# Performance work log

Measured on AMD Instinct MI355X. Metric: run time of the kernel, lower is better.

The kernel has to match this reference:

```python
import jax, jax.numpy as jnp
import numpy as np

VARIANCE = (0.1, 0.2)
NUM_CLASSES = 81
NEGPOS_RATIO = 3
THRESH = 0.5


def point_form(b):
    # cxcywh -> xyxy
    return jnp.concatenate([b[:, :2] - b[:, 2:] / 2, b[:, :2] + b[:, 2:] / 2], axis=1)


def iou_jaccard(box1, box2):
    # box1: [G,4] xyxy, box2: [P,4] xyxy -> [G,P]
    lt = jnp.maximum(box1[:, None, :2], box2[None, :, :2])
    rb = jnp.minimum(box1[:, None, 2:], box2[None, :, 2:])
    wh = jnp.clip(rb - lt, 0.0)
    inter = wh[..., 0] * wh[..., 1]
    a1 = ((box1[:, 2] - box1[:, 0]) * (box1[:, 3] - box1[:, 1]))[:, None]
    a2 = ((box2[:, 2] - box2[:, 0]) * (box2[:, 3] - box2[:, 1]))[None, :]
    return inter / (a1 + a2 - inter)


def encode(matched, priors):
    # matched: [P,4] xyxy gt per prior; priors: [P,4] cxcywh
    cxcy = (matched[:, :2] + matched[:, 2:]) / 2 - priors[:, :2]
    cxcy = cxcy / (priors[:, 2:] * VARIANCE[0])
    wh = jnp.log((matched[:, 2:] - matched[:, :2]) / priors[:, 2:]) / VARIANCE[1]
    return jnp.concatenate([cxcy, wh], axis=1)


def assign_one(gt_box, gt_class, priors):
    ov = iou_jaccard(gt_box, point_form(priors))  # [G,P]
    best_iou = ov.max(axis=0)                      # [P]
    best_gt = ov.argmax(axis=0)                    # [P]
    best_prior = ov.argmax(axis=1)                 # [G]
    best_iou = best_iou.at[best_prior].set(2.0)    # force-keep each gt's best prior
    loc_t = encode(gt_box[best_gt], priors)
    cls = gt_class[best_gt] + 1
    cls = jnp.where(best_iou < THRESH, 0, cls)
    return loc_t, cls


def setup_inputs() -> dict:
    key = jax.random.key(0)
    ks = jax.random.split(key, 7)
    B, P, C, G = 64, 8732, NUM_CLASSES, 16
    loc_p = jax.random.normal(ks[0], (B, P, 4), jnp.float32)
    class_p = jax.random.normal(ks[1], (B, P, C), jnp.float32)
    p_cxcy = jax.random.uniform(ks[2], (P, 2), jnp.float32, 0.05, 0.95)
    p_wh = jax.random.uniform(ks[3], (P, 2), jnp.float32, 0.05, 0.5)
    priors = jnp.concatenate([p_cxcy, p_wh], axis=1)
    xy1 = jax.random.uniform(ks[4], (B, G, 2), jnp.float32, 0.0, 0.6)
    wh = jax.random.uniform(ks[5], (B, G, 2), jnp.float32, 0.05, 0.35)
    gt_box = jnp.concatenate([xy1, xy1 + wh], axis=-1)
    gt_class = jax.random.randint(ks[6], (B, G), 0, C - 1, jnp.int32)
    return {"loc_p": loc_p, "class_p": class_p, "priors": priors,
            "gt_box": gt_box, "gt_class": gt_class}


def reference(loc_p, class_p, priors, gt_box, gt_class):
    B, P, _ = loc_p.shape
    loc_t, class_t = jax.vmap(lambda b, c: assign_one(b, c, priors))(gt_box, gt_class)
    loc_t = jax.lax.stop_gradient(loc_t)
    class_t = jax.lax.stop_gradient(class_t)

    pos = class_t > 0                                 # [B,P]
    num_pos = pos.sum(axis=1, keepdims=True)          # [B,1]

    # masked smooth-L1 (sum reduction), beta=1
    diff = jnp.abs(loc_p - loc_t)
    sl1 = jnp.where(diff < 1.0, 0.5 * diff * diff, diff - 0.5)
    loss_l = jnp.sum(sl1 * pos[..., None].astype(loc_p.dtype))

    # per-prior cross entropy
    logp = jax.nn.log_softmax(class_p, axis=-1)       # [B,P,C]
    ce = -jnp.take_along_axis(logp, class_t[..., None], axis=-1)[..., 0]  # [B,P]

    # hard negative mining: rank by CE with positives zeroed out
    loss_gt = jnp.where(pos, 0.0, ce)
    sort_idx = jnp.argsort(-loss_gt, axis=1)
    idx_rank = jnp.argsort(sort_idx, axis=1)
    num_neg = jnp.minimum(NEGPOS_RATIO * num_pos, P - 1)
    neg = idx_rank < num_neg

    sel = pos | neg
    loss_c = jnp.sum(jnp.where(sel, ce, 0.0))

    N = num_pos.sum().astype(loc_p.dtype)
    return loss_l / N, loss_c / N
```

## Files before the change

### kernel.cpp

```cpp
#include <hip/hip_runtime.h>
#include <math.h>

#define SPLIT 16

__device__ __forceinline__ float wave_sum(float v) {
  for (int m = 32; m > 0; m >>= 1) v += __shfl_xor(v, m, 64);
  return v;
}
__device__ __forceinline__ int wave_sum_i(int v) {
  for (int m = 32; m > 0; m >>= 1) v += __shfl_xor(v, m, 64);
  return v;
}
__device__ __forceinline__ unsigned long long wave_max_key(unsigned long long k) {
  for (int m = 32; m > 0; m >>= 1) {
    unsigned lo = (unsigned)k, hi = (unsigned)(k >> 32);
    lo = __shfl_xor(lo, m, 64); hi = __shfl_xor(hi, m, 64);
    unsigned long long o = ((unsigned long long)hi << 32) | lo;
    if (o > k) k = o;
  }
  return k;
}

__global__ __launch_bounds__(256) void match1_kernel(
    const float* __restrict__ priors, const float* __restrict__ gt_box,
    float* __restrict__ best_iou, int* __restrict__ best_gt,
    unsigned long long* __restrict__ gt_best,
    int P, int G, int chunk)
{
  const int b = blockIdx.y;
  const int p0 = blockIdx.x * chunk;
  const int p1 = min(p0 + chunk, P);
  const int tid = threadIdx.x, lane = tid & 63;

  __shared__ float sgx1[64], sgy1[64], sgx2[64], sgy2[64], sga[64];
  for (int g = tid; g < G; g += 256) {
    float x1 = gt_box[((size_t)b * G + g) * 4 + 0];
    float y1 = gt_box[((size_t)b * G + g) * 4 + 1];
    float x2 = gt_box[((size_t)b * G + g) * 4 + 2];
    float y2 = gt_box[((size_t)b * G + g) * 4 + 3];
    sgx1[g] = x1; sgy1[g] = y1; sgx2[g] = x2; sgy2[g] = y2;
    sga[g] = (x2 - x1) * (y2 - y1);
  }
  __syncthreads();

  for (int g0 = 0; g0 < G; g0 += 16) {
    const int gc = min(16, G - g0);
    unsigned long long bkey[16];
#pragma unroll
    for (int gg = 0; gg < 16; ++gg) bkey[gg] = 0ull;

    for (int p = p0 + tid; p < p1; p += 256) {
      const size_t ip = (size_t)b * P + p;
      float pcx = priors[p * 4 + 0], pcy = priors[p * 4 + 1];
      float pw = priors[p * 4 + 2], ph = priors[p * 4 + 3];
      float px1 = pcx - pw * 0.5f, py1 = pcy - ph * 0.5f;
      float px2 = pcx + pw * 0.5f, py2 = pcy + ph * 0.5f;
      float pa = (px2 - px1) * (py2 - py1);
      float bv; int bg;
      if (g0 == 0) { bv = -INFINITY; bg = 0; }
      else { bv = best_iou[ip]; bg = best_gt[ip]; }
#pragma unroll
      for (int gg = 0; gg < 16; ++gg) {
        if (gg < gc) {
          int g = g0 + gg;
          float ix = fmaxf(fminf(sgx2[g], px2) - fmaxf(sgx1[g], px1), 0.f);
          float iy = fmaxf(fminf(sgy2[g], py2) - fmaxf(sgy1[g], py1), 0.f);
          float inter = ix * iy;
          float ov = inter / (sga[g] + pa - inter);
          if (ov > bv) { bv = ov; bg = g; }
          unsigned long long key =
              ((unsigned long long)__float_as_uint(ov) << 32) |
              (unsigned)(0x7FFFFFFF - p);
          if (key > bkey[gg]) bkey[gg] = key;
        }
      }
      best_iou[ip] = bv;
      best_gt[ip] = bg;
    }

#pragma unroll
    for (int gg = 0; gg < 16; ++gg) {
      if (gg < gc) {
        unsigned long long k = wave_max_key(bkey[gg]);
        if (lane == 0 && k)
          atomicMax(&gt_best[(size_t)b * G + g0 + gg], k);
      }
    }
  }
}

__global__ void force_kernel(const unsigned long long* __restrict__ gt_best,
                             float* __restrict__ best_iou, int P, int G)
{
  const int b = blockIdx.x, t = threadIdx.x;
  if (t < G) {
    unsigned long long k = gt_best[(size_t)b * G + t];
    int p = 0x7FFFFFFF - (int)(unsigned)(k & 0xFFFFFFFFu);
    if (p >= 0 && p < P) best_iou[(size_t)b * P + p] = 2.0f;
  }
}

__global__ __launch_bounds__(256) void match3_kernel(
    const float* __restrict__ priors, const float* __restrict__ gt_box,
    const int* __restrict__ gt_class, const float* __restrict__ loc_p,
    const float* __restrict__ best_iou, const int* __restrict__ best_gt,
    int* __restrict__ class_t, int* __restrict__ num_pos_arr,
    float* __restrict__ loss_l_accum, int* __restrict__ n_total,
    int P, int G, int chunk)
{
  const int b = blockIdx.y;
  const int p0 = blockIdx.x * chunk;
  const int p1 = min(p0 + chunk, P);
  const int tid = threadIdx.x, lane = tid & 63, wv = tid >> 6;

  __shared__ float sgx1[64], sgy1[64], sgx2[64], sgy2[64];
  __shared__ int sgtc[64];
  __shared__ float sredf[4];
  __shared__ int sredi[4];

  for (int g = tid; g < G; g += 256) {
    sgx1[g] = gt_box[((size_t)b * G + g) * 4 + 0];
    sgy1[g] = gt_box[((size_t)b * G + g) * 4 + 1];
    sgx2[g] = gt_box[((size_t)b * G + g) * 4 + 2];
    sgy2[g] = gt_box[((size_t)b * G + g) * 4 + 3];
    sgtc[g] = gt_class[(size_t)b * G + g];
  }
  __syncthreads();

  int cnt = 0; float lsum = 0.f;
  for (int p = p0 + tid; p < p1; p += 256) {
    const size_t ip = (size_t)b * P + p;
    float bi = best_iou[ip];
    int bg = best_gt[ip];
    int ct = (bi < 0.5f) ? 0 : (sgtc[bg] + 1);
    class_t[ip] = ct;
    if (ct > 0) {
      cnt++;
      float pcx = priors[p * 4 + 0], pcy = priors[p * 4 + 1];
      float pw = priors[p * 4 + 2], ph = priors[p * 4 + 3];
      float mx1 = sgx1[bg], my1 = sgy1[bg], mx2 = sgx2[bg], my2 = sgy2[bg];
      float tx = ((mx1 + mx2) * 0.5f - pcx) / (pw * 0.1f);
      float ty = ((my1 + my2) * 0.5f - pcy) / (ph * 0.1f);
      float tw = logf((mx2 - mx1) / pw) / 0.2f;
      float th = logf((my2 - my1) / ph) / 0.2f;
      const float* lp = loc_p + ip * 4;
      float t0[4] = {tx, ty, tw, th};
#pragma unroll
      for (int j = 0; j < 4; ++j) {
        float d = fabsf(lp[j] - t0[j]);
        lsum += (d < 1.f) ? 0.5f * d * d : d - 0.5f;
      }
    }
  }
  lsum = wave_sum(lsum);
  cnt = wave_sum_i(cnt);
  if (lane == 0) { sredf[wv] = lsum; sredi[wv] = cnt; }
  __syncthreads();
  if (tid == 0) {
    float ls = sredf[0] + sredf[1] + sredf[2] + sredf[3];
    int c = sredi[0] + sredi[1] + sredi[2] + sredi[3];
    if (c) { atomicAdd(&num_pos_arr[b], c); atomicAdd(n_total, c); }
    if (ls != 0.f) atomicAdd(loss_l_accum, ls);
  }
}

#define CE_ROWS 128
#define CE_MAXC 96
__global__ __launch_bounds__(CE_ROWS) void ce_kernel(
    const float* __restrict__ class_p,
    const int* __restrict__ class_t,
    float* __restrict__ loss_gt,
    float* __restrict__ loss_c_accum,
    int C, long long nrows)
{
  __shared__ float4 sbuf4[CE_ROWS * CE_MAXC / 4];
  float* srow = (float*)sbuf4;
  __shared__ float sred[CE_ROWS / 64];

  const long long row0 = (long long)blockIdx.x * CE_ROWS;
  const int rows_valid = (int)(nrows - row0 < CE_ROWS ? nrows - row0 : CE_ROWS);
  const int totalf = rows_valid * C;
  const float* gsrc = class_p + row0 * C;
  const int total4 = totalf >> 2;
  const float4* gsrc4 = (const float4*)gsrc;
  for (int i = threadIdx.x; i < total4; i += CE_ROWS) sbuf4[i] = gsrc4[i];
  for (int i = (total4 << 2) + threadIdx.x; i < totalf; i += CE_ROWS) srow[i] = gsrc[i];
  __syncthreads();

  const int t = threadIdx.x, lane = t & 63, wv = t >> 6;
  float pc = 0.f;
  if (t < rows_valid) {
    const float* x = srow + t * C;
    float m = -INFINITY;
    for (int c = 0; c < C; ++c) m = fmaxf(m, x[c]);
    float s = 0.f;
    for (int c = 0; c < C; ++c) s += __expf(x[c] - m);
    const long long row = row0 + t;
    const int ct = class_t[row];
    const float ce = m + __logf(s) - x[ct];
    float lg;
    if (ct > 0) { lg = 0.f; pc = ce; }
    else        { lg = fmaxf(ce, 0.f); }
    loss_gt[row] = lg;
  }
  pc = wave_sum(pc);
  if (lane == 0) sred[wv] = pc;
  __syncthreads();
  if (t == 0) {
    float s = 0.f;
#pragma unroll
    for (int j = 0; j < CE_ROWS / 64; ++j) s += sred[j];
    if (s != 0.f) atomicAdd(loss_c_accum, s);
  }
}

__global__ __launch_bounds__(1024) void topk_kernel(
    const float* __restrict__ loss_gt, const int* __restrict__ num_pos_arr,
    float* __restrict__ loss_c_accum, int P, int negpos_ratio)
{
  extern __shared__ float sv[];
  __shared__ int scnt[16];
  __shared__ float ssum[16];

  const int b = blockIdx.x;
  const int tid = threadIdx.x;
  const int lane = tid & 63, wv = tid >> 6;
  for (int i = tid; i < P; i += 1024) sv[i] = loss_gt[(size_t)b * P + i];
  __syncthreads();
  const int np = num_pos_arr[b];
  const int k = min(negpos_ratio * np, P - 1);
  if (k <= 0) return;

  unsigned u = 0;
  for (int bit = 30; bit >= 0; --bit) {
    unsigned cand = u | (1u << bit);
    int cnt = 0;
    for (int i = tid; i < P; i += 1024) cnt += (__float_as_uint(sv[i]) >= cand) ? 1 : 0;
    cnt = wave_sum_i(cnt);
    if (lane == 0) scnt[wv] = cnt;
    __syncthreads();
    int tot = 0;
#pragma unroll
    for (int j = 0; j < 16; ++j) tot += scnt[j];
    if (tot >= k) u = cand;
    __syncthreads();
  }
  const float vk = __uint_as_float(u);
  int cgt = 0; float sgt = 0.f;
  for (int i = tid; i < P; i += 1024) {
    float v = sv[i];
    if (__float_as_uint(v) > u) { cgt += 1; sgt += v; }
  }
  cgt = wave_sum_i(cgt);
  sgt = wave_sum(sgt);
  if (lane == 0) { scnt[wv] = cgt; ssum[wv] = sgt; }
  __syncthreads();
  if (tid == 0) {
    int cg = 0; float sg = 0.f;
#pragma unroll
    for (int j = 0; j < 16; ++j) { cg += scnt[j]; sg += ssum[j]; }
    atomicAdd(loss_c_accum, sg + vk * (float)(k - cg));
  }
}

__global__ void finalize_kernel(const float* __restrict__ lla,
                                const float* __restrict__ lca,
                                const int* __restrict__ nt,
                                float* __restrict__ out)
{
  if (threadIdx.x == 0 && blockIdx.x == 0) {
    float N = (float)(*nt);
    out[0] = lla[0] / N;
    out[1] = lca[0] / N;
  }
}

extern "C" void kernel_launch(void* const* d_in, const int* in_sizes, int n_in,
                              void* d_out, int out_size, void* d_ws, size_t ws_size,
                              hipStream_t stream) {
  const float* loc_p   = (const float*)d_in[0];
  const float* class_p = (const float*)d_in[1];
  const float* priors  = (const float*)d_in[2];
  const float* gt_box  = (const float*)d_in[3];
  const int*   gt_cls  = (const int*)d_in[4];

  const int P = in_sizes[2] / 4;
  const int B = in_sizes[0] / (4 * P);
  const int C = (int)((long long)in_sizes[1] / ((long long)B * P));
  const int G = in_sizes[4] / B;
  const long long BP = (long long)B * P;

  char* w = (char*)d_ws;
  float* best_iou = (float*)w; w += BP * 4;
  int*   bst_gt   = (int*)w;   w += BP * 4;
  int*   cls_t    = (int*)w;   w += BP * 4;
  float* loss_gt  = (float*)w; w += BP * 4;
  char* zbase = w;
  float* lla = (float*)w;  w += 4;
  float* lca = (float*)w;  w += 4;
  int*   ntot = (int*)w;   w += 4;
  w += 4;
  unsigned long long* gt_best = (unsigned long long*)w; w += (size_t)B * G * 8;
  int* num_pos = (int*)w;  w += (size_t)B * 4;
  const size_t zbytes = (size_t)(w - zbase);

  hipMemsetAsync(zbase, 0, zbytes, stream);

  const int chunk = (P + SPLIT - 1) / SPLIT;
  match1_kernel<<<dim3(SPLIT, B), 256, 0, stream>>>(
      priors, gt_box, best_iou, bst_gt, gt_best, P, G, chunk);
  force_kernel<<<B, 64, 0, stream>>>(gt_best, best_iou, P, G);
  match3_kernel<<<dim3(SPLIT, B), 256, 0, stream>>>(
      priors, gt_box, gt_cls, loc_p, best_iou, bst_gt, cls_t,
      num_pos, lla, ntot, P, G, chunk);

  const long long nrows = BP;
  const int nblocks = (int)((nrows + CE_ROWS - 1) / CE_ROWS);
  ce_kernel<<<nblocks, CE_ROWS, 0, stream>>>(class_p, cls_t, loss_gt, lca, C, nrows);

  topk_kernel<<<B, 1024, (size_t)P * sizeof(float), stream>>>(
      loss_gt, num_pos, lca, P, 3);

  finalize_kernel<<<1, 1, 0, stream>>>(lla, lca, ntot, (float*)d_out);
}
```

Baseline: 416.3 us.

## Fuse force, match3 and CE into one kernel; fold finalize into topk

Removes the separate force and match3 kernels. Their work (forced-prior check, class target, localization loss, positive count) now happens inside a cross-entropy kernel specialized for 81 classes, which uses four threads per row and keeps a 64-row tile in shared memory. The top-k kernel keeps each thread's values in registers instead of shared memory. A last-block-done atomic counter replaces the finalize kernel. This cuts launches and the class_t round trip through memory, at the cost of a per-row loop over G to check forced priors.

```diff
diff --git a/kernel.cpp b/kernel.cpp
--- a/kernel.cpp
+++ b/kernel.cpp
@@ -2,6 +2,9 @@
 #include <math.h>
 
 #define SPLIT 16
+#define CER 64
+#define CEC 81
+#define TKJ 16
 
 __device__ __forceinline__ float wave_sum(float v) {
   for (int m = 32; m > 0; m >>= 1) v += __shfl_xor(v, m, 64);
@@ -89,189 +92,247 @@
   }
 }
 
-__global__ void force_kernel(const unsigned long long* __restrict__ gt_best,
-                             float* __restrict__ best_iou, int P, int G)
+__global__ __launch_bounds__(256) void ce81_kernel(
+    const float* __restrict__ class_p, const float* __restrict__ priors,
+    const float* __restrict__ gt_box, const int* __restrict__ gt_class,
+    const float* __restrict__ loc_p,
+    const float* __restrict__ best_iou, const int* __restrict__ best_gt,
+    const unsigned long long* __restrict__ gt_best,
+    float* __restrict__ loss_gt, int* __restrict__ num_pos_arr,
+    float* __restrict__ lla, float* __restrict__ lca, int* __restrict__ ntot,
+    int P, int G)
 {
-  const int b = blockIdx.x, t = threadIdx.x;
-  if (t < G) {
-    unsigned long long k = gt_best[(size_t)b * G + t];
-    int p = 0x7FFFFFFF - (int)(unsigned)(k & 0xFFFFFFFFu);
-    if (p >= 0 && p < P) best_iou[(size_t)b * P + p] = 2.0f;
-  }
-}
-
-__global__ __launch_bounds__(256) void match3_kernel(
-    const float* __restrict__ priors, const float* __restrict__ gt_box,
-    const int* __restrict__ gt_class, const float* __restrict__ loc_p,
+  __shared__ float srow[CER * CEC];
+  __shared__ float4 sgb[64];
+  __shared__ int sgtc[64], sforce[64];
+  __shared__ float sbi[CER];
+  __shared__ int sbg[CER];
+  __shared__ float sr_pc[4], sr_ls[4];
+  __shared__ int sr_cnt[4];
+
+  const int b = blockIdx.y;
+  const int p0 = blockIdx.x * CER;
+  const int rows = min(CER, P - p0);
+  const int tid = threadIdx.x;
+
+  const float* gsrc = class_p + ((size_t)b * P + p0) * CEC;
+  const int nf = rows * CEC;
+  if ((((unsigned long long)(uintptr_t)gsrc) & 15ull) == 0) {
+    const int n4 = nf >> 2;
+    for (int i = tid; i < n4; i += 256)
+      ((float4*)srow)[i] = ((const float4*)gsrc)[i];
+    for (int i = (n4 << 2) + tid; i < nf; i += 256) srow[i] = gsrc[i];
+  } else {
+    for (int i = tid; i < nf; i += 256) srow[i] = gsrc[i];
+  }
+  for (int i = tid; i < rows; i += 256) {
+    sbi[i] = best_iou[(size_t)b * P + p0 + i];
+    sbg[i] = best_gt[(size_t)b * P + p0 + i];
+  }
+  if (tid < G) {
+    sgb[tid] = ((const float4*)gt_box)[(size_t)b * G + tid];
+    sgtc[tid] = gt_class[(size_t)b * G + tid];
+    unsigned long long k = gt_best[(size_t)b * G + tid];
+    sforce[tid] = 0x7FFFFFFF - (int)(unsigned)(k & 0xFFFFFFFFu);
+  }
+  __syncthreads();
+
+  const int r = tid >> 2, q = tid & 3;
+  const int lane = tid & 63, wv = tid >> 6;
+  float posce = 0.f, lsum = 0.f; int cnt = 0;
+
+  if (r < rows) {
+    const float* x = srow + r * CEC;
+    float m = -INFINITY;
+    for (int c = q; c < CEC; c += 4) m = fmaxf(m, x[c]);
+    m = fmaxf(m, __shfl_xor(m, 1, 64));
+    m = fmaxf(m, __shfl_xor(m, 2, 64));
+    float s = 0.f;
+    for (int c = q; c < CEC; c += 4) s += __expf(x[c] - m);
+    s += __shfl_xor(s, 1, 64);
+    s += __shfl_xor(s, 2, 64);
+
+    if (q == 0) {
+      const int p = p0 + r;
+      const size_t row = (size_t)b * P + p;
+      const float bi = sbi[r];
+      const int bg = sbg[r];
+      bool forced = false;
+      for (int g = 0; g < G; ++g) forced |= (p == sforce[g]);
+      const bool pos = forced || (bi >= 0.5f);
+      const int ct = pos ? (sgtc[bg] + 1) : 0;
+      const float ce = m + __logf(s) - x[ct];
+      float lg;
+      if (pos) {
+        lg = 0.f; posce = ce; cnt = 1;
+        float pcx = priors[p * 4 + 0], pcy = priors[p * 4 + 1];
+        float pw = priors[p * 4 + 2], ph = priors[p * 4 + 3];
+        float4 gb = sgb[bg];
+        float tx = ((gb.x + gb.z) * 0.5f - pcx) / (pw * 0.1f);
+        float ty = ((gb.y + gb.w) * 0.5f - pcy) / (ph * 0.1f);
+        float tw = logf((gb.z - gb.x) / pw) / 0.2f;
+        float th = logf((gb.w - gb.y) / ph) / 0.2f;
+        const float* lp = loc_p + row * 4;
+        float t0[4] = {tx, ty, tw, th};
+#pragma unroll
+        for (int j = 0; j < 4; ++j) {
+          float d = fabsf(lp[j] - t0[j]);
+          lsum += (d < 1.f) ? 0.5f * d * d : d - 0.5f;
+        }
+      } else {
+        lg = fmaxf(ce, 0.f);
+      }
+      loss_gt[row] = lg;
+    }
+  }
+
+  posce = wave_sum(posce);
+  lsum = wave_sum(lsum);
+  cnt = wave_sum_i(cnt);
+  if (lane == 0) { sr_pc[wv] = posce; sr_ls[wv] = lsum; sr_cnt[wv] = cnt; }
+  __syncthreads();
+  if (tid == 0) {
+    float pc = sr_pc[0] + sr_pc[1] + sr_pc[2] + sr_pc[3];
+    float ls = sr_ls[0] + sr_ls[1] + sr_ls[2] + sr_ls[3];
+    int c = sr_cnt[0] + sr_cnt[1] + sr_cnt[2] + sr_cnt[3];
+    if (c) { atomicAdd(&num_pos_arr[b], c); atomicAdd(ntot, c); }
+    if (ls != 0.f) atomicAdd(lla, ls);
+    if (pc != 0.f) atomicAdd(lca, pc);
+  }
+}
+
+__global__ void ce_generic_kernel(
+    const float* __restrict__ class_p, const float* __restrict__ priors,
+    const float* __restrict__ gt_box, const int* __restrict__ gt_class,
+    const float* __restrict__ loc_p,
     const float* __restrict__ best_iou, const int* __restrict__ best_gt,
-    int* __restrict__ class_t, int* __restrict__ num_pos_arr,
-    float* __restrict__ loss_l_accum, int* __restrict__ n_total,
-    int P, int G, int chunk)
+    const unsigned long long* __restrict__ gt_best,
+    float* __restrict__ loss_gt, int* __restrict__ num_pos_arr,
+    float* __restrict__ lla, float* __restrict__ lca, int* __restrict__ ntot,
+    int P, int G, int C)
 {
+  __shared__ float4 sgb[64];
+  __shared__ int sgtc[64], sforce[64];
+  __shared__ float sr_pc[4], sr_ls[4];
+  __shared__ int sr_cnt[4];
   const int b = blockIdx.y;
-  const int p0 = blockIdx.x * chunk;
-  const int p1 = min(p0 + chunk, P);
+  const int p = blockIdx.x * 256 + threadIdx.x;
   const int tid = threadIdx.x, lane = tid & 63, wv = tid >> 6;
-
-  __shared__ float sgx1[64], sgy1[64], sgx2[64], sgy2[64];
-  __shared__ int sgtc[64];
-  __shared__ float sredf[4];
-  __shared__ int sredi[4];
-
-  for (int g = tid; g < G; g += 256) {
-    sgx1[g] = gt_box[((size_t)b * G + g) * 4 + 0];
-    sgy1[g] = gt_box[((size_t)b * G + g) * 4 + 1];
-    sgx2[g] = gt_box[((size_t)b * G + g) * 4 + 2];
-    sgy2[g] = gt_box[((size_t)b * G + g) * 4 + 3];
-    sgtc[g] = gt_class[(size_t)b * G + g];
-  }
-  __syncthreads();
-
-  int cnt = 0; float lsum = 0.f;
-  for (int p = p0 + tid; p < p1; p += 256) {
-    const size_t ip = (size_t)b * P + p;
-    float bi = best_iou[ip];
-    int bg = best_gt[ip];
-    int ct = (bi < 0.5f) ? 0 : (sgtc[bg] + 1);
-    class_t[ip] = ct;
-    if (ct > 0) {
-      cnt++;
+  if (tid < G) {
+    sgb[tid] = ((const float4*)gt_box)[(size_t)b * G + tid];
+    sgtc[tid] = gt_class[(size_t)b * G + tid];
+    unsigned long long k = gt_best[(size_t)b * G + tid];
+    sforce[tid] = 0x7FFFFFFF - (int)(unsigned)(k & 0xFFFFFFFFu);
+  }
+  __syncthreads();
+  float posce = 0.f, lsum = 0.f; int cnt = 0;
+  if (p < P) {
+    const size_t row = (size_t)b * P + p;
+    const float* x = class_p + row * C;
+    float m = -INFINITY;
+    for (int c = 0; c < C; ++c) m = fmaxf(m, x[c]);
+    float s = 0.f;
+    for (int c = 0; c < C; ++c) s += __expf(x[c] - m);
+    const float bi = best_iou[row];
+    const int bg = best_gt[row];
+    bool forced = false;
+    for (int g = 0; g < G; ++g) forced |= (p == sforce[g]);
+    const bool pos = forced || (bi >= 0.5f);
+    const int ct = pos ? (sgtc[bg] + 1) : 0;
+    const float ce = m + __logf(s) - x[ct];
+    float lg;
+    if (pos) {
+      lg = 0.f; posce = ce; cnt = 1;
       float pcx = priors[p * 4 + 0], pcy = priors[p * 4 + 1];
       float pw = priors[p * 4 + 2], ph = priors[p * 4 + 3];
-      float mx1 = sgx1[bg], my1 = sgy1[bg], mx2 = sgx2[bg], my2 = sgy2[bg];
-      float tx = ((mx1 + mx2) * 0.5f - pcx) / (pw * 0.1f);
-      float ty = ((my1 + my2) * 0.5f - pcy) / (ph * 0.1f);
-      float tw = logf((mx2 - mx1) / pw) / 0.2f;
-      float th = logf((my2 - my1) / ph) / 0.2f;
-      const float* lp = loc_p + ip * 4;
-      float t0[4] = {tx, ty, tw, th};
+      float4 gb = sgb[bg];
+      float t0[4] = {((gb.x + gb.z) * 0.5f - pcx) / (pw * 0.1f),
+                     ((gb.y + gb.w) * 0.5f - pcy) / (ph * 0.1f),
+                     logf((gb.z - gb.x) / pw) / 0.2f,
+                     logf((gb.w - gb.y) / ph) / 0.2f};
+      const float* lp = loc_p + row * 4;
 #pragma unroll
       for (int j = 0; j < 4; ++j) {
         float d = fabsf(lp[j] - t0[j]);
         lsum += (d < 1.f) ? 0.5f * d * d : d - 0.5f;
       }
-    }
-  }
-  lsum = wave_sum(lsum);
-  cnt = wave_sum_i(cnt);
-  if (lane == 0) { sredf[wv] = lsum; sredi[wv] = cnt; }
+    } else lg = fmaxf(ce, 0.f);
+    loss_gt[row] = lg;
+  }
+  posce = wave_sum(posce); lsum = wave_sum(lsum); cnt = wave_sum_i(cnt);
+  if (lane == 0) { sr_pc[wv] = posce; sr_ls[wv] = lsum; sr_cnt[wv] = cnt; }
   __syncthreads();
   if (tid == 0) {
-    float ls = sredf[0] + sredf[1] + sredf[2] + sredf[3];
-    int c = sredi[0] + sredi[1] + sredi[2] + sredi[3];
-    if (c) { atomicAdd(&num_pos_arr[b], c); atomicAdd(n_total, c); }
-    if (ls != 0.f) atomicAdd(loss_l_accum, ls);
-  }
-}
-
-#define CE_ROWS 128
-#define CE_MAXC 96
-__global__ __launch_bounds__(CE_ROWS) void ce_kernel(
-    const float* __restrict__ class_p,
-    const int* __restrict__ class_t,
-    float* __restrict__ loss_gt,
-    float* __restrict__ loss_c_accum,
-    int C, long long nrows)
+    float pc = sr_pc[0] + sr_pc[1] + sr_pc[2] + sr_pc[3];
+    float ls = sr_ls[0] + sr_ls[1] + sr_ls[2] + sr_ls[3];
+    int c = sr_cnt[0] + sr_cnt[1] + sr_cnt[2] + sr_cnt[3];
+    if (c) { atomicAdd(&num_pos_arr[b], c); atomicAdd(ntot, c); }
+    if (ls != 0.f) atomicAdd(lla, ls);
+    if (pc != 0.f) atomicAdd(lca, pc);
+  }
+}
+
+__global__ __launch_bounds__(1024) void topk_fin_kernel(
+    const float* __restrict__ loss_gt, const int* __restrict__ num_pos_arr,
+    float* __restrict__ lla, float* __restrict__ lca, int* __restrict__ ntot,
+    int* __restrict__ done, float* __restrict__ out,
+    int P, int negpos_ratio, int B)
 {
-  __shared__ float4 sbuf4[CE_ROWS * CE_MAXC / 4];
-  float* srow = (float*)sbuf4;
-  __shared__ float sred[CE_ROWS / 64];
-
-  const long long row0 = (long long)blockIdx.x * CE_ROWS;
-  const int rows_valid = (int)(nrows - row0 < CE_ROWS ? nrows - row0 : CE_ROWS);
-  const int totalf = rows_valid * C;
-  const float* gsrc = class_p + row0 * C;
-  const int total4 = totalf >> 2;
-  const float4* gsrc4 = (const float4*)gsrc;
-  for (int i = threadIdx.x; i < total4; i += CE_ROWS) sbuf4[i] = gsrc4[i];
-  for (int i = (total4 << 2) + threadIdx.x; i < totalf; i += CE_ROWS) srow[i] = gsrc[i];
-  __syncthreads();
-
-  const int t = threadIdx.x, lane = t & 63, wv = t >> 6;
-  float pc = 0.f;
-  if (t < rows_valid) {
-    const float* x = srow + t * C;
-    float m = -INFINITY;
-    for (int c = 0; c < C; ++c) m = fmaxf(m, x[c]);
-    float s = 0.f;
-    for (int c = 0; c < C; ++c) s += __expf(x[c] - m);
-    const long long row = row0 + t;
-    const int ct = class_t[row];
-    const float ce = m + __logf(s) - x[ct];
-    float lg;
-    if (ct > 0) { lg = 0.f; pc = ce; }
-    else        { lg = fmaxf(ce, 0.f); }
-    loss_gt[row] = lg;
-  }
-  pc = wave_sum(pc);
-  if (lane == 0) sred[wv] = pc;
-  __syncthreads();
-  if (t == 0) {
-    float s = 0.f;
-#pragma unroll
-    for (int j = 0; j < CE_ROWS / 64; ++j) s += sred[j];
-    if (s != 0.f) atomicAdd(loss_c_accum, s);
-  }
-}
-
-__global__ __launch_bounds__(1024) void topk_kernel(
-    const float* __restrict__ loss_gt, const int* __restrict__ num_pos_arr,
-    float* __restrict__ loss_c_accum, int P, int negpos_ratio)
-{
-  extern __shared__ float sv[];
   __shared__ int scnt[16];
   __shared__ float ssum[16];
-
   const int b = blockIdx.x;
-  const int tid = threadIdx.x;
-  const int lane = tid & 63, wv = tid >> 6;
-  for (int i = tid; i < P; i += 1024) sv[i] = loss_gt[(size_t)b * P + i];
-  __syncthreads();
+  const int tid = threadIdx.x, lane = tid & 63, wv = tid >> 6;
   const int np = num_pos_arr[b];
   const int k = min(negpos_ratio * np, P - 1);
-  if (k <= 0) return;
-
-  unsigned u = 0;
-  for (int bit = 30; bit >= 0; --bit) {
-    unsigned cand = u | (1u << bit);
-    int cnt = 0;
-    for (int i = tid; i < P; i += 1024) cnt += (__float_as_uint(sv[i]) >= cand) ? 1 : 0;
-    cnt = wave_sum_i(cnt);
-    if (lane == 0) scnt[wv] = cnt;
+
+  if (k > 0) {
+    unsigned uv[TKJ];
+#pragma unroll
+    for (int j = 0; j < TKJ; ++j) {
+      int i = tid + j * 1024;
+      uv[j] = (i < P) ? __float_as_uint(loss_gt[(size_t)b * P + i]) : 0u;
+    }
+    unsigned u = 0;
+    for (int bit = 30; bit >= 0; --bit) {
+      unsigned cand = u | (1u << bit);
+      int cnt = 0;
+#pragma unroll
+      for (int j = 0; j < TKJ; ++j) cnt += (uv[j] >= cand) ? 1 : 0;
+      cnt = wave_sum_i(cnt);
+      if (lane == 0) scnt[wv] = cnt;
+      __syncthreads();
+      int tot = 0;
+#pragma unroll
+      for (int j = 0; j < 16; ++j) tot += scnt[j];
+      if (tot >= k) u = cand;
+      __syncthreads();
+    }
+    const float vk = __uint_as_float(u);
+    int cgt = 0; float sgt = 0.f;
+#pragma unroll
+    for (int j = 0; j < TKJ; ++j)
+      if (uv[j] > u) { cgt++; sgt += __uint_as_float(uv[j]); }
+    cgt = wave_sum_i(cgt); sgt = wave_sum(sgt);
+    if (lane == 0) { scnt[wv] = cgt; ssum[wv] = sgt; }
     __syncthreads();
-    int tot = 0;
-#pragma unroll
-    for (int j = 0; j < 16; ++j) tot += scnt[j];
-    if (tot >= k) u = cand;
-    __syncthreads();
-  }
-  const float vk = __uint_as_float(u);
-  int cgt = 0; float sgt = 0.f;
-  for (int i = tid; i < P; i += 1024) {
-    float v = sv[i];
-    if (__float_as_uint(v) > u) { cgt += 1; sgt += v; }
-  }
-  cgt = wave_sum_i(cgt);
-  sgt = wave_sum(sgt);
-  if (lane == 0) { scnt[wv] = cgt; ssum[wv] = sgt; }
-  __syncthreads();
+    if (tid == 0) {
+      int cg = 0; float sg = 0.f;
+#pragma unroll
+      for (int j = 0; j < 16; ++j) { cg += scnt[j]; sg += ssum[j]; }
+      atomicAdd(lca, sg + vk * (float)(k - cg));
+    }
+  }
+
   if (tid == 0) {
-    int cg = 0; float sg = 0.f;
-#pragma unroll
-    for (int j = 0; j < 16; ++j) { cg += scnt[j]; sg += ssum[j]; }
-    atomicAdd(loss_c_accum, sg + vk * (float)(k - cg));
-  }
-}
-
-__global__ void finalize_kernel(const float* __restrict__ lla,
-                                const float* __restrict__ lca,
-                                const int* __restrict__ nt,
-                                float* __restrict__ out)
-{
-  if (threadIdx.x == 0 && blockIdx.x == 0) {
-    float N = (float)(*nt);
-    out[0] = lla[0] / N;
-    out[1] = lca[0] / N;
+    __threadfence();
+    int old = atomicAdd(done, 1);
+    if (old == B - 1) {
+      float N = (float)atomicAdd(ntot, 0);
+      float L = atomicAdd(lla, 0.f);
+      float Cc = atomicAdd(lca, 0.f);
+      out[0] = L / N;
+      out[1] = Cc / N;
+    }
   }
 }
 
@@ -293,13 +354,12 @@
   char* w = (char*)d_ws;
   float* best_iou = (float*)w; w += BP * 4;
   int*   bst_gt   = (int*)w;   w += BP * 4;
-  int*   cls_t    = (int*)w;   w += BP * 4;
   float* loss_gt  = (float*)w; w += BP * 4;
   char* zbase = w;
-  float* lla = (float*)w;  w += 4;
-  float* lca = (float*)w;  w += 4;
+  float* lla  = (float*)w; w += 4;
+  float* lca  = (float*)w; w += 4;
   int*   ntot = (int*)w;   w += 4;
-  w += 4;
+  int*   done = (int*)w;   w += 4;
   unsigned long long* gt_best = (unsigned long long*)w; w += (size_t)B * G * 8;
   int* num_pos = (int*)w;  w += (size_t)B * 4;
   const size_t zbytes = (size_t)(w - zbase);
@@ -309,17 +369,17 @@
   const int chunk = (P + SPLIT - 1) / SPLIT;
   match1_kernel<<<dim3(SPLIT, B), 256, 0, stream>>>(
       priors, gt_box, best_iou, bst_gt, gt_best, P, G, chunk);
-  force_kernel<<<B, 64, 0, stream>>>(gt_best, best_iou, P, G);
-  match3_kernel<<<dim3(SPLIT, B), 256, 0, stream>>>(
-      priors, gt_box, gt_cls, loc_p, best_iou, bst_gt, cls_t,
-      num_pos, lla, ntot, P, G, chunk);
-
-  const long long nrows = BP;
-  const int nblocks = (int)((nrows + CE_ROWS - 1) / CE_ROWS);
-  ce_kernel<<<nblocks, CE_ROWS, 0, stream>>>(class_p, cls_t, loss_gt, lca, C, nrows);
-
-  topk_kernel<<<B, 1024, (size_t)P * sizeof(float), stream>>>(
-      loss_gt, num_pos, lca, P, 3);
-
-  finalize_kernel<<<1, 1, 0, stream>>>(lla, lca, ntot, (float*)d_out);
-}
+
+  if (C == CEC) {
+    ce81_kernel<<<dim3((P + CER - 1) / CER, B), 256, 0, stream>>>(
+        class_p, priors, gt_box, gt_cls, loc_p, best_iou, bst_gt, gt_best,
+        loss_gt, num_pos, lla, lca, ntot, P, G);
+  } else {
+    ce_generic_kernel<<<dim3((P + 255) / 256, B), 256, 0, stream>>>(
+        class_p, priors, gt_box, gt_cls, loc_p, best_iou, bst_gt, gt_best,
+        loss_gt, num_pos, lla, lca, ntot, P, G, C);
+  }
+
+  topk_fin_kernel<<<B, 1024, 0, stream>>>(
+      loss_gt, num_pos, lla, lca, ntot, done, (float*)d_out, P, 3, B);
+}
```

After: 566.0 us. +36.0%, slower.
